# Kernel optimization log

Hardware: AMD Instinct MI355X
Metric: run time of the kernel (lower is better)

## Reference

```python
import jax, jax.numpy as jnp
import numpy as np

N, E = 50000, 800000          # nodes, edges
IN, HID, H, OUT = 128, 64, 4, 64  # in_size, hid_size, num_heads, out_size
NEG_SLOPE = 0.2               # DGL GATConv default leaky_relu slope
EPS = 1e-5                    # LayerNorm eps


def setup_inputs() -> dict:
    key = jax.random.key(0)
    ks = jax.random.split(key, 20)
    f32 = jnp.float32

    def nrm(k, shape, fan_in):
        return jax.random.normal(k, shape, f32) * (1.0 / np.sqrt(fan_in))

    inp = {}
    inp['feats'] = jax.random.normal(ks[0], (N, IN), f32)
    inp['src'] = jax.random.randint(ks[1], (E,), 0, N, jnp.int32)
    inp['dst'] = jnp.sort(jax.random.randint(ks[2], (E,), 0, N, jnp.int32))
    # GATConv 0: in -> H*HID, bias=False
    inp['W0'] = nrm(ks[3], (IN, H * HID), IN)
    inp['al0'] = nrm(ks[4], (H, HID), HID)
    inp['ar0'] = nrm(ks[5], (H, HID), HID)
    # residual linear 0
    inp['resw0'] = nrm(ks[6], (IN, HID), IN)
    inp['resb0'] = jnp.zeros((HID,), f32)
    # LayerNorm 0
    inp['g0'] = jnp.ones((HID,), f32)
    inp['b0'] = jnp.zeros((HID,), f32)
    # GATConv 1: hid -> H*HID (out_linear=True so last layer is hid->hid)
    inp['W1'] = nrm(ks[7], (HID, H * HID), HID)
    inp['al1'] = nrm(ks[8], (H, HID), HID)
    inp['ar1'] = nrm(ks[9], (H, HID), HID)
    # residual linear 1
    inp['resw1'] = nrm(ks[10], (HID, HID), HID)
    inp['resb1'] = jnp.zeros((HID,), f32)
    # LayerNorm 1
    inp['g1'] = jnp.ones((HID,), f32)
    inp['b1'] = jnp.zeros((HID,), f32)
    # final prediction head
    inp['predw'] = nrm(ks[11], (HID, OUT), HID)
    inp['predb'] = jnp.zeros((OUT,), f32)
    return inp


def _gat_conv(h, W, al, ar, src, dst):
    """DGL GATConv (bias=False, no internal residual), returns [N,H,Dh]."""
    Hh, Dh = al.shape
    fs = (h @ W).reshape(-1, Hh, Dh)              # [N,H,Dh]
    el = jnp.einsum('nhd,hd->nh', fs, al)         # [N,H]
    er = jnp.einsum('nhd,hd->nh', fs, ar)
    e = jax.nn.leaky_relu(el[src] + er[dst], NEG_SLOPE)  # [E,H]
    # edge softmax over incoming edges of each destination node
    emax = jax.ops.segment_max(e, dst, num_segments=N, indices_are_sorted=True)
    a = jnp.exp(e - emax[dst])
    asum = jax.ops.segment_sum(a, dst, num_segments=N, indices_are_sorted=True)
    a = a / asum[dst]
    msg = a[:, :, None] * fs[src]                 # [E,H,Dh]
    return jax.ops.segment_sum(msg, dst, num_segments=N, indices_are_sorted=True)


def _layer_norm(x, g, b):
    mu = jnp.mean(x, axis=-1, keepdims=True)
    var = jnp.mean(jnp.square(x - mu), axis=-1, keepdims=True)
    return (x - mu) / jnp.sqrt(var + EPS) * g + b


def reference(feats, src, dst, W0, al0, ar0, resw0, resb0, g0, b0,
              W1, al1, ar1, resw1, resb1, g1, b1, predw, predb):
    # layer 0: conv.mean(heads) + residual linear, then LN + ReLU (dropout=0)
    h = _gat_conv(feats, W0, al0, ar0, src, dst).mean(axis=1) + (feats @ resw0 + resb0)
    h = jax.nn.relu(_layer_norm(h, g0, b0))
    # layer 1 (out_linear=True -> same treatment)
    h = _gat_conv(h, W1, al1, ar1, src, dst).mean(axis=1) + (h @ resw1 + resb1)
    h = jax.nn.relu(_layer_norm(h, g1, b1))
    # final prediction
    return h @ predw + predb
```

## Files before the change

### kernel.cpp

```cpp
#include <hip/hip_runtime.h>
#include <hip/hip_bf16.h>

#define N_NODES 50000
#define E_EDGES 800000
#define NH 4
#define NEG_SLOPE 0.2f
#define LN_EPS 1e-5f

__device__ __forceinline__ unsigned short f2bf(float x) {
    __hip_bfloat16 h = __float2bfloat16(x);
    unsigned short u;
    __builtin_memcpy(&u, &h, sizeof(u));
    return u;
}

__global__ void k_rowptr(const int* __restrict__ dst, int* __restrict__ rp) {
    int d = blockIdx.x * blockDim.x + threadIdx.x;
    if (d > N_NODES) return;
    int lo = 0, hi = E_EDGES;
    while (lo < hi) {
        int mid = (lo + hi) >> 1;
        if (dst[mid] < d) lo = mid + 1; else hi = mid;
    }
    rp[d] = lo;
}

template<int K>
__global__ __launch_bounds__(256) void k_gemm(
    const float* __restrict__ hin, const float* __restrict__ W,
    const float* __restrict__ al, const float* __restrict__ ar,
    const float* __restrict__ resw, const float* __restrict__ resb,
    __hip_bfloat16* __restrict__ fs, float* __restrict__ el,
    float* __restrict__ er, float* __restrict__ resid)
{
    __shared__ __align__(16) float hl[K * 16];
    const int n0 = blockIdx.x * 16;
    const int t  = threadIdx.x;

    for (int idx = t; idx < 16 * K; idx += 256) {
        int n = idx / K, k = idx - n * K;
        hl[k * 16 + n] = hin[(long long)(n0 + n) * K + k];
    }
    __syncthreads();

    const int c  = t & 63;
    const int g  = t >> 6;
    const int c4 = 4 * c;

    float4 acc[4];
    #pragma unroll
    for (int j = 0; j < 4; ++j) acc[j] = make_float4(0.f, 0.f, 0.f, 0.f);

    #pragma unroll 4
    for (int k = 0; k < K; ++k) {
        const float4 w4 = *(const float4*)&W[k * 256 + c4];
        const float4 a4 = *(const float4*)&hl[k * 16 + 4 * g];
        acc[0].x = fmaf(w4.x, a4.x, acc[0].x);
        acc[0].y = fmaf(w4.y, a4.x, acc[0].y);
        acc[0].z = fmaf(w4.z, a4.x, acc[0].z);
        acc[0].w = fmaf(w4.w, a4.x, acc[0].w);
        acc[1].x = fmaf(w4.x, a4.y, acc[1].x);
        acc[1].y = fmaf(w4.y, a4.y, acc[1].y);
        acc[1].z = fmaf(w4.z, a4.y, acc[1].z);
        acc[1].w = fmaf(w4.w, a4.y, acc[1].w);
        acc[2].x = fmaf(w4.x, a4.z, acc[2].x);
        acc[2].y = fmaf(w4.y, a4.z, acc[2].y);
        acc[2].z = fmaf(w4.z, a4.z, acc[2].z);
        acc[2].w = fmaf(w4.w, a4.z, acc[2].w);
        acc[3].x = fmaf(w4.x, a4.w, acc[3].x);
        acc[3].y = fmaf(w4.y, a4.w, acc[3].y);
        acc[3].z = fmaf(w4.z, a4.w, acc[3].z);
        acc[3].w = fmaf(w4.w, a4.w, acc[3].w);
    }

    #pragma unroll
    for (int j = 0; j < 4; ++j) {
        const int node = n0 + 4 * g + j;
        ushort4 pk;
        pk.x = f2bf(acc[j].x);
        pk.y = f2bf(acc[j].y);
        pk.z = f2bf(acc[j].z);
        pk.w = f2bf(acc[j].w);
        *(ushort4*)&fs[(long long)node * 256 + c4] = pk;
    }

    {
        const float4 al4 = *(const float4*)&al[c4];
        const float4 ar4 = *(const float4*)&ar[c4];
        float e_l[4], e_r[4];
        #pragma unroll
        for (int j = 0; j < 4; ++j) {
            e_l[j] = acc[j].x * al4.x + acc[j].y * al4.y
                   + acc[j].z * al4.z + acc[j].w * al4.w;
            e_r[j] = acc[j].x * ar4.x + acc[j].y * ar4.y
                   + acc[j].z * ar4.z + acc[j].w * ar4.w;
        }
        #pragma unroll
        for (int o = 8; o > 0; o >>= 1) {
            #pragma unroll
            for (int j = 0; j < 4; ++j) {
                e_l[j] += __shfl_xor(e_l[j], o, 64);
                e_r[j] += __shfl_xor(e_r[j], o, 64);
            }
        }
        if ((c & 15) == 0) {
            const int h = c >> 4;
            #pragma unroll
            for (int j = 0; j < 4; ++j) {
                const int node = n0 + 4 * g + j;
                el[node * NH + h] = e_l[j];
                er[node * NH + h] = e_r[j];
            }
        }
    }

    float r[4] = {0.f, 0.f, 0.f, 0.f};
    for (int k = 0; k < K; ++k) {
        float w = resw[k * 64 + c];
        #pragma unroll
        for (int j = 0; j < 4; ++j)
            r[j] = fmaf(hl[k * 16 + g + 4 * j], w, r[j]);
    }
    float bb = resb[c];
    #pragma unroll
    for (int j = 0; j < 4; ++j)
        resid[(long long)(n0 + g + 4 * j) * 64 + c] = r[j] + bb;
}

template<bool FINAL>
__global__ __launch_bounds__(256) void k_agg(
    const int* __restrict__ rp, const int* __restrict__ src,
    const unsigned int* __restrict__ fs_u,
    const float* __restrict__ el, const float* __restrict__ er,
    const float* __restrict__ resid,
    const float* __restrict__ g, const float* __restrict__ b,
    const float* __restrict__ predw, const float* __restrict__ predb,
    float* __restrict__ out)
{
    __shared__ __align__(16) float aw[4][64][4];
    __shared__ int   sjw[4][64];
    __shared__ float ylds[4][64];

    const int t    = threadIdx.x;
    const int wv   = t >> 6;
    const int lane = t & 63;
    const int d    = blockIdx.x * 4 + wv;
    const int l    = lane & 31;
    const int h2   = lane >> 5;
    const int hh   = l >> 3;

    const int start = rp[d], end = rp[d + 1];
    const float4 er4 = *(const float4*)(er + d * NH);

    float4 s4 = make_float4(0.f, 0.f, 0.f, 0.f);
    float acc[8];
    #pragma unroll
    for (int i = 0; i < 8; ++i) acc[i] = 0.f;

    for (int cs = start; cs < end; cs += 64) {
        const int cnt = min(64, end - cs);
        int   sj = 0;
        float4 a4 = make_float4(0.f, 0.f, 0.f, 0.f);
        if (lane < cnt) {
            sj = src[cs + lane];
            const float4 el4 = *(const float4*)(el + sj * NH);
            float ex = el4.x + er4.x; ex = ex > 0.f ? ex : NEG_SLOPE * ex;
            float ey = el4.y + er4.y; ey = ey > 0.f ? ey : NEG_SLOPE * ey;
            float ez = el4.z + er4.z; ez = ez > 0.f ? ez : NEG_SLOPE * ez;
            float ew = el4.w + er4.w; ew = ew > 0.f ? ew : NEG_SLOPE * ew;
            a4.x = __expf(ex); a4.y = __expf(ey);
            a4.z = __expf(ez); a4.w = __expf(ew);
            s4.x += a4.x; s4.y += a4.y; s4.z += a4.z; s4.w += a4.w;
        }
        sjw[wv][lane] = sj;
        *(float4*)&aw[wv][lane][0] = a4;
        for (int jj = 0; jj < cnt; jj += 2) {
            const int j2 = jj + h2;
            if (j2 < cnt) {
                const float w = aw[wv][j2][hh];
                const int   s = sjw[wv][j2];
                const uint4 u = *((const uint4*)(fs_u + (size_t)s * 128) + l);
                acc[0] = fmaf(w, __uint_as_float(u.x << 16),         acc[0]);
                acc[1] = fmaf(w, __uint_as_float(u.x & 0xffff0000u), acc[1]);
                acc[2] = fmaf(w, __uint_as_float(u.y << 16),         acc[2]);
                acc[3] = fmaf(w, __uint_as_float(u.y & 0xffff0000u), acc[3]);
                acc[4] = fmaf(w, __uint_as_float(u.z << 16),         acc[4]);
                acc[5] = fmaf(w, __uint_as_float(u.z & 0xffff0000u), acc[5]);
                acc[6] = fmaf(w, __uint_as_float(u.w << 16),         acc[6]);
                acc[7] = fmaf(w, __uint_as_float(u.w & 0xffff0000u), acc[7]);
            }
        }
    }

    #pragma unroll
    for (int i = 0; i < 8; ++i) acc[i] += __shfl_xor(acc[i], 32);

    #pragma unroll
    for (int o = 32; o > 0; o >>= 1) {
        s4.x += __shfl_xor(s4.x, o);
        s4.y += __shfl_xor(s4.y, o);
        s4.z += __shfl_xor(s4.z, o);
        s4.w += __shfl_xor(s4.w, o);
    }
    const float rsx = s4.x > 0.f ? 1.f / s4.x : 0.f;
    const float rsy = s4.y > 0.f ? 1.f / s4.y : 0.f;
    const float rsz = s4.z > 0.f ? 1.f / s4.z : 0.f;
    const float rsw = s4.w > 0.f ? 1.f / s4.w : 0.f;
    const float rsh = hh == 0 ? rsx : hh == 1 ? rsy : hh == 2 ? rsz : rsw;
    #pragma unroll
    for (int i = 0; i < 8; ++i) acc[i] *= rsh;

    #pragma unroll
    for (int i = 0; i < 8; ++i) {
        acc[i] += __shfl_xor(acc[i], 8);
        acc[i] += __shfl_xor(acc[i], 16);
    }

    const int c0 = 8 * (l & 7);
    const float4 r0 = *(const float4*)(resid + (size_t)d * 64 + c0);
    const float4 r1 = *(const float4*)(resid + (size_t)d * 64 + c0 + 4);
    float v[8];
    v[0] = 0.25f * acc[0] + r0.x;  v[1] = 0.25f * acc[1] + r0.y;
    v[2] = 0.25f * acc[2] + r0.z;  v[3] = 0.25f * acc[3] + r0.w;
    v[4] = 0.25f * acc[4] + r1.x;  v[5] = 0.25f * acc[5] + r1.y;
    v[6] = 0.25f * acc[6] + r1.z;  v[7] = 0.25f * acc[7] + r1.w;

    float p = 0.f, p2 = 0.f;
    #pragma unroll
    for (int i = 0; i < 8; ++i) { p += v[i]; p2 += v[i] * v[i]; }
    #pragma unroll
    for (int o = 4; o > 0; o >>= 1) {
        p  += __shfl_xor(p,  o);
        p2 += __shfl_xor(p2, o);
    }
    const float mu  = p * (1.f / 64.f);
    const float var = p2 * (1.f / 64.f) - mu * mu;
    const float inv = 1.f / sqrtf(fmaxf(var, 0.f) + LN_EPS);

    const float4 g0v = *(const float4*)(g + c0);
    const float4 g1v = *(const float4*)(g + c0 + 4);
    const float4 b0v = *(const float4*)(b + c0);
    const float4 b1v = *(const float4*)(b + c0 + 4);
    float y[8];
    y[0] = fmaxf((v[0] - mu) * inv * g0v.x + b0v.x, 0.f);
    y[1] = fmaxf((v[1] - mu) * inv * g0v.y + b0v.y, 0.f);
    y[2] = fmaxf((v[2] - mu) * inv * g0v.z + b0v.z, 0.f);
    y[3] = fmaxf((v[3] - mu) * inv * g0v.w + b0v.w, 0.f);
    y[4] = fmaxf((v[4] - mu) * inv * g1v.x + b1v.x, 0.f);
    y[5] = fmaxf((v[5] - mu) * inv * g1v.y + b1v.y, 0.f);
    y[6] = fmaxf((v[6] - mu) * inv * g1v.z + b1v.z, 0.f);
    y[7] = fmaxf((v[7] - mu) * inv * g1v.w + b1v.w, 0.f);

    if (!FINAL) {
        if (lane < 8) {
            float4 o0 = make_float4(y[0], y[1], y[2], y[3]);
            float4 o1 = make_float4(y[4], y[5], y[6], y[7]);
            *(float4*)(out + (size_t)d * 64 + 8 * lane)     = o0;
            *(float4*)(out + (size_t)d * 64 + 8 * lane + 4) = o1;
        }
    } else {
        if (lane < 8) {
            #pragma unroll
            for (int i = 0; i < 8; ++i) ylds[wv][8 * lane + i] = y[i];
        }
        float o = predb[lane];
        #pragma unroll 4
        for (int k = 0; k < 64; ++k)
            o = fmaf(ylds[wv][k], predw[k * 64 + lane], o);
        out[(size_t)d * 64 + lane] = o;
    }
}

extern "C" void kernel_launch(void* const* d_in, const int* in_sizes, int n_in,
                              void* d_out, int out_size, void* d_ws, size_t ws_size,
                              hipStream_t stream)
{
    const float* feats = (const float*)d_in[0];
    const int*   src   = (const int*)  d_in[1];
    const int*   dst   = (const int*)  d_in[2];
    const float* W0    = (const float*)d_in[3];
    const float* al0   = (const float*)d_in[4];
    const float* ar0   = (const float*)d_in[5];
    const float* resw0 = (const float*)d_in[6];
    const float* resb0 = (const float*)d_in[7];
    const float* g0    = (const float*)d_in[8];
    const float* b0    = (const float*)d_in[9];
    const float* W1    = (const float*)d_in[10];
    const float* al1   = (const float*)d_in[11];
    const float* ar1   = (const float*)d_in[12];
    const float* resw1 = (const float*)d_in[13];
    const float* resb1 = (const float*)d_in[14];
    const float* g1    = (const float*)d_in[15];
    const float* b1    = (const float*)d_in[16];
    const float* predw = (const float*)d_in[17];
    const float* predb = (const float*)d_in[18];
    float* out = (float*)d_out;

    char* ws = (char*)d_ws;
    int*   rp = (int*)ws;
    __hip_bfloat16* fs = (__hip_bfloat16*)(ws + 200192);
    float* el    = (float*)((char*)fs + (size_t)N_NODES * 256 * 2);
    float* er    = el + (size_t)N_NODES * 4;
    float* resid = er + (size_t)N_NODES * 4;
    float* h1    = resid + (size_t)N_NODES * 64;

    k_rowptr<<<(N_NODES + 1 + 255) / 256, 256, 0, stream>>>(dst, rp);

    k_gemm<128><<<N_NODES / 16, 256, 0, stream>>>(
        feats, W0, al0, ar0, resw0, resb0, fs, el, er, resid);
    k_agg<false><<<N_NODES / 4, 256, 0, stream>>>(
        rp, src, (const unsigned int*)fs, el, er, resid, g0, b0,
        nullptr, nullptr, h1);

    k_gemm<64><<<N_NODES / 16, 256, 0, stream>>>(
        h1, W1, al1, ar1, resw1, resb1, fs, el, er, resid);
    k_agg<true><<<N_NODES / 4, 256, 0, stream>>>(
        rp, src, (const unsigned int*)fs, el, er, resid, g1, b1,
        predw, predb, out);
}
```

Baseline: 387.2 us.

## Enlarge GEMM node tile to 32 and fuse residual projection into main loop

The projection GEMM now processes 32 nodes per block instead of 16, with 8 nodes per thread, so each weight load is reused across twice as many nodes. The residual linear is folded into the same k-loop, dropping the second pass over shared memory. The shared tile is padded to 33 columns to avoid bank conflicts, and the tail is clamped with bounds checks. It also adds an unroll hint to the aggregation inner loop. The costs are higher register pressure and fewer blocks in flight, and the GEMM is likely a small share of total time next to the edge aggregation.

Result: faster. 367.4 us (-5.1%).

```diff
diff --git a/kernel.cpp b/kernel.cpp
--- a/kernel.cpp
+++ b/kernel.cpp
@@ -33,13 +33,14 @@
     __hip_bfloat16* __restrict__ fs, float* __restrict__ el,
     float* __restrict__ er, float* __restrict__ resid)
 {
-    __shared__ __align__(16) float hl[K * 16];
-    const int n0 = blockIdx.x * 16;
+    __shared__ float hl[K * 33];
+    const int n0 = blockIdx.x * 32;
     const int t  = threadIdx.x;
 
-    for (int idx = t; idx < 16 * K; idx += 256) {
+    for (int idx = t; idx < 32 * K; idx += 256) {
         int n = idx / K, k = idx - n * K;
-        hl[k * 16 + n] = hin[(long long)(n0 + n) * K + k];
+        int node = min(n0 + n, N_NODES - 1);
+        hl[k * 33 + n] = hin[(long long)node * K + k];
     }
     __syncthreads();
 
@@ -47,49 +48,60 @@
     const int g  = t >> 6;
     const int c4 = 4 * c;
 
-    float4 acc[4];
-    #pragma unroll
-    for (int j = 0; j < 4; ++j) acc[j] = make_float4(0.f, 0.f, 0.f, 0.f);
-
-    #pragma unroll 4
+    float4 acc[8];
+    float  r[8];
+    #pragma unroll
+    for (int j = 0; j < 8; ++j) {
+        acc[j] = make_float4(0.f, 0.f, 0.f, 0.f);
+        r[j] = 0.f;
+    }
+
+    #pragma unroll 2
     for (int k = 0; k < K; ++k) {
         const float4 w4 = *(const float4*)&W[k * 256 + c4];
-        const float4 a4 = *(const float4*)&hl[k * 16 + 4 * g];
-        acc[0].x = fmaf(w4.x, a4.x, acc[0].x);
-        acc[0].y = fmaf(w4.y, a4.x, acc[0].y);
-        acc[0].z = fmaf(w4.z, a4.x, acc[0].z);
-        acc[0].w = fmaf(w4.w, a4.x, acc[0].w);
-        acc[1].x = fmaf(w4.x, a4.y, acc[1].x);
-        acc[1].y = fmaf(w4.y, a4.y, acc[1].y);
-        acc[1].z = fmaf(w4.z, a4.y, acc[1].z);
-        acc[1].w = fmaf(w4.w, a4.y, acc[1].w);
-        acc[2].x = fmaf(w4.x, a4.z, acc[2].x);
-        acc[2].y = fmaf(w4.y, a4.z, acc[2].y);
-        acc[2].z = fmaf(w4.z, a4.z, acc[2].z);
-        acc[2].w = fmaf(w4.w, a4.z, acc[2].w);
-        acc[3].x = fmaf(w4.x, a4.w, acc[3].x);
-        acc[3].y = fmaf(w4.y, a4.w, acc[3].y);
-        acc[3].z = fmaf(w4.z, a4.w, acc[3].z);
-        acc[3].w = fmaf(w4.w, a4.w, acc[3].w);
-    }
-
-    #pragma unroll
-    for (int j = 0; j < 4; ++j) {
-        const int node = n0 + 4 * g + j;
-        ushort4 pk;
-        pk.x = f2bf(acc[j].x);
-        pk.y = f2bf(acc[j].y);
-        pk.z = f2bf(acc[j].z);
-        pk.w = f2bf(acc[j].w);
-        *(ushort4*)&fs[(long long)node * 256 + c4] = pk;
+        const float  rw = resw[k * 64 + c];
+        float a[8];
+        #pragma unroll
+        for (int j = 0; j < 8; ++j) a[j] = hl[k * 33 + 8 * g + j];
+        #pragma unroll
+        for (int j = 0; j < 8; ++j) {
+            acc[j].x = fmaf(w4.x, a[j], acc[j].x);
+            acc[j].y = fmaf(w4.y, a[j], acc[j].y);
+            acc[j].z = fmaf(w4.z, a[j], acc[j].z);
+            acc[j].w = fmaf(w4.w, a[j], acc[j].w);
+            r[j]     = fmaf(rw,   a[j], r[j]);
+        }
+    }
+
+    #pragma unroll
+    for (int j = 0; j < 8; ++j) {
+        const int node = n0 + 8 * g + j;
+        if (node < N_NODES) {
+            ushort4 pk;
+            pk.x = f2bf(acc[j].x);
+            pk.y = f2bf(acc[j].y);
+            pk.z = f2bf(acc[j].z);
+            pk.w = f2bf(acc[j].w);
+            *(ushort4*)&fs[(long long)node * 256 + c4] = pk;
+        }
+    }
+
+    {
+        const float bb = resb[c];
+        #pragma unroll
+        for (int j = 0; j < 8; ++j) {
+            const int node = n0 + 8 * g + j;
+            if (node < N_NODES)
+                resid[(long long)node * 64 + c] = r[j] + bb;
+        }
     }
 
     {
         const float4 al4 = *(const float4*)&al[c4];
         const float4 ar4 = *(const float4*)&ar[c4];
-        float e_l[4], e_r[4];
-        #pragma unroll
-        for (int j = 0; j < 4; ++j) {
+        float e_l[8], e_r[8];
+        #pragma unroll
+        for (int j = 0; j < 8; ++j) {
             e_l[j] = acc[j].x * al4.x + acc[j].y * al4.y
                    + acc[j].z * al4.z + acc[j].w * al4.w;
             e_r[j] = acc[j].x * ar4.x + acc[j].y * ar4.y
@@ -98,7 +110,7 @@
         #pragma unroll
         for (int o = 8; o > 0; o >>= 1) {
             #pragma unroll
-            for (int j = 0; j < 4; ++j) {
+            for (int j = 0; j < 8; ++j) {
                 e_l[j] += __shfl_xor(e_l[j], o, 64);
                 e_r[j] += __shfl_xor(e_r[j], o, 64);
             }
@@ -106,25 +118,15 @@
         if ((c & 15) == 0) {
             const int h = c >> 4;
             #pragma unroll
-            for (int j = 0; j < 4; ++j) {
-                const int node = n0 + 4 * g + j;
-                el[node * NH + h] = e_l[j];
-                er[node * NH + h] = e_r[j];
+            for (int j = 0; j < 8; ++j) {
+                const int node = n0 + 8 * g + j;
+                if (node < N_NODES) {
+                    el[node * NH + h] = e_l[j];
+                    er[node * NH + h] = e_r[j];
+                }
             }
         }
     }
-
-    float r[4] = {0.f, 0.f, 0.f, 0.f};
-    for (int k = 0; k < K; ++k) {
-        float w = resw[k * 64 + c];
-        #pragma unroll
-        for (int j = 0; j < 4; ++j)
-            r[j] = fmaf(hl[k * 16 + g + 4 * j], w, r[j]);
-    }
-    float bb = resb[c];
-    #pragma unroll
-    for (int j = 0; j < 4; ++j)
-        resid[(long long)(n0 + g + 4 * j) * 64 + c] = r[j] + bb;
 }
 
 template<bool FINAL>
@@ -174,6 +176,7 @@
         }
         sjw[wv][lane] = sj;
         *(float4*)&aw[wv][lane][0] = a4;
+        #pragma unroll 4
         for (int jj = 0; jj < cnt; jj += 2) {
             const int j2 = jj + h2;
             if (j2 < cnt) {
@@ -306,13 +309,13 @@
 
     k_rowptr<<<(N_NODES + 1 + 255) / 256, 256, 0, stream>>>(dst, rp);
 
-    k_gemm<128><<<N_NODES / 16, 256, 0, stream>>>(
+    k_gemm<128><<<(N_NODES + 31) / 32, 256, 0, stream>>>(
         feats, W0, al0, ar0, resw0, resb0, fs, el, er, resid);
     k_agg<false><<<N_NODES / 4, 256, 0, stream>>>(
         rp, src, (const unsigned int*)fs, el, er, resid, g0, b0,
         nullptr, nullptr, h1);
 
-    k_gemm<64><<<N_NODES / 16, 256, 0, stream>>>(
+    k_gemm<64><<<(N_NODES + 31) / 32, 256, 0, stream>>>(
         h1, W1, al1, ar1, resw1, resb1, fs, el, er, resid);
     k_agg<true><<<N_NODES / 4, 256, 0, stream>>>(
         rp, src, (const unsigned int*)fs, el, er, resid, g1, b1,
```
